# Optimization experiments

Measured on AMD Instinct MI355X. Metric: run time of the kernel, lower is better.

Reference implementation:

```python
import jax, jax.numpy as jnp
import numpy as np

# ---- fixed problem dimensions ----
B, S, T = 64, 200, 32          # batch of sequences, trees per seq, nodes per tree
V, E, C = 50000, 128, 128      # vocab, embedding_dim, encode_dim
H, OUT = 100, 104              # GRU hidden, output_dim
N = B * S * T                  # total nodes
D_MAX = 5                      # max depth of a 32-node complete binary tree


def setup_inputs() -> dict:
    key = jax.random.key(0)
    ks = jax.random.split(key, 16)
    # --- tree structure: every tree is a complete binary tree with T nodes ---
    local_parent = np.array([0] + [(i - 1) // 2 for i in range(1, T)], dtype=np.int64)
    local_depth = np.array([int(np.floor(np.log2(i + 1))) for i in range(T)], dtype=np.int64)
    num_trees = B * S
    offsets = np.arange(num_trees, dtype=np.int64) * T
    node_parent = (offsets[:, None] + local_parent[None, :]).reshape(-1)
    node_depth = np.tile(local_depth, num_trees)
    node_tree = np.repeat(np.arange(num_trees, dtype=np.int64), T)
    node_tokens = jax.random.randint(ks[0], (N,), 0, V, dtype=jnp.int64)
    sc = 0.05
    inp = {
        "node_tokens": node_tokens,
        "node_parent": jnp.asarray(node_parent),
        "node_tree": jnp.asarray(node_tree),
        "node_depth": jnp.asarray(node_depth),
        "emb": jax.random.normal(ks[1], (V, E), jnp.float32) * sc,
        "w_lin": jax.random.normal(ks[2], (C, E), jnp.float32) * sc,
        "b_lin": jnp.zeros((C,), jnp.float32),
        "w_ih_f": jax.random.normal(ks[3], (3 * H, C), jnp.float32) * sc,
        "w_hh_f": jax.random.normal(ks[4], (3 * H, H), jnp.float32) * sc,
        "b_ih_f": jnp.zeros((3 * H,), jnp.float32),
        "b_hh_f": jnp.zeros((3 * H,), jnp.float32),
        "w_ih_b": jax.random.normal(ks[5], (3 * H, C), jnp.float32) * sc,
        "w_hh_b": jax.random.normal(ks[6], (3 * H, H), jnp.float32) * sc,
        "b_ih_b": jnp.zeros((3 * H,), jnp.float32),
        "b_hh_b": jnp.zeros((3 * H,), jnp.float32),
        "fc_w": jax.random.normal(ks[7], (OUT, 2 * H), jnp.float32) * sc,
        "fc_b": jnp.zeros((OUT,), jnp.float32),
    }
    return inp


def _gru(x_sbc, w_ih, w_hh, b_ih, b_hh):
    """Torch-convention GRU over leading time axis. x_sbc: [S, B, C] -> [S, B, H]."""
    h0 = jnp.zeros((x_sbc.shape[1], w_hh.shape[1]), x_sbc.dtype)

    def step(h, xt):
        gx = xt @ w_ih.T + b_ih
        gh = h @ w_hh.T + b_hh
        xr, xz, xn = jnp.split(gx, 3, axis=-1)
        hr, hz, hn = jnp.split(gh, 3, axis=-1)
        r = jax.nn.sigmoid(xr + hr)
        z = jax.nn.sigmoid(xz + hz)
        n = jnp.tanh(xn + r * hn)
        h_new = (1.0 - z) * n + z * h
        return h_new, h_new

    _, hs = jax.lax.scan(step, h0, x_sbc)
    return hs


def reference(node_tokens, node_parent, node_tree, node_depth,
              emb, w_lin, b_lin,
              w_ih_f, w_hh_f, b_ih_f, b_hh_f,
              w_ih_b, w_hh_b, b_ih_b, b_hh_b,
              fc_w, fc_b):
    # per-node contribution: W * emb(token) + b   (recursion base of hidden_state)
    c = emb[node_tokens] @ w_lin.T + b_lin               # [N, C]
    # level-batched bottom-up scatter-add: h(node) = c(node) + sum(h(children))
    h = c
    for d in range(D_MAX, 0, -1):
        mask = (node_depth == d)[:, None]
        h = h.at[node_parent].add(jnp.where(mask, h, 0.0))
    # per-tree max pool over all node hidden states (TreeEncoder output)
    tree_vec = jax.ops.segment_max(h, node_tree, num_segments=B * S)  # [B*S, C]
    x = tree_vec.reshape(B, S, C)
    # bidirectional GRU (batch_first in torch; scan over time here)
    x_t = jnp.transpose(x, (1, 0, 2))                    # [S, B, C]
    fwd = _gru(x_t, w_ih_f, w_hh_f, b_ih_f, b_hh_f)      # [S, B, H]
    bwd = _gru(x_t[::-1], w_ih_b, w_hh_b, b_ih_b, b_hh_b)[::-1]
    gru_out = jnp.concatenate([fwd, bwd], axis=-1)       # [S, B, 2H]
    pool = gru_out.max(axis=0)                           # [B, 2H] (max over time)
    return pool @ fc_w.T + fc_b                          # [B, OUT]
```

## Files before the change

### kernel.cpp

```cpp
#include <hip/hip_runtime.h>
#include <hip/hip_bf16.h>
#include <math.h>

#define BB 64
#define SS 200
#define TT 32
#define VV 50000
#define EE 128
#define CC 128
#define HH 100
#define G3 300
#define OUTD 104
#define NTREE (BB*SS)

typedef __attribute__((ext_vector_type(4))) float f32x4;
typedef _Float16 f16x8 __attribute__((ext_vector_type(8)));

#define L2E  1.4426950408889634f
#define NL2E (-1.4426950408889634f)
#define TL2E 2.8853900817779268f

#define BAR() asm volatile("s_waitcnt lgkmcnt(0)\n\ts_barrier" ::: "memory")


__global__ __launch_bounds__(256) void k0_prep(const float* __restrict__ w_lin,
                                               const float* __restrict__ w_ih_f,
                                               const float* __restrict__ w_ih_b,
                                               const float* __restrict__ emb,
                                               _Float16* __restrict__ wl,
                                               _Float16* __restrict__ k2b,
                                               _Float16* __restrict__ emb16) {
    const int tid  = threadIdx.x;
    const int wave = tid >> 6;
    const int lane = tid & 63;
    const int r = lane & 15;
    const int q = lane >> 4;
    if (blockIdx.x == 0) {
#pragma unroll
        for (int nt = 0; nt < 2; ++nt)
#pragma unroll
            for (int kt = 0; kt < 4; ++kt) {
                const int n = wave * 32 + nt * 16 + r;
                const float* src = w_lin + (long)n * EE + kt * 32 + q * 8;
                f16x8 f;
#pragma unroll
                for (int e = 0; e < 8; ++e) f[e] = (_Float16)src[e];
                *(f16x8*)&wl[(size_t)((((wave * 2 + nt) * 4 + kt) * 64) + lane) * 8] = f;
            }
    } else if (blockIdx.x <= 10) {
        const int nb = blockIdx.x - 1;
        const int n = nb * 64 + wave * 16 + r;
        const int dir = (n >= 320) ? 1 : 0;
        const int j = n - dir * 320;
        const int jj = (j < G3) ? j : 0;
        const float* w = dir ? w_ih_b : w_ih_f;
#pragma unroll
        for (int kt = 0; kt < 4; ++kt) {
            const float* src = w + (long)jj * EE + kt * 32 + q * 8;
            f16x8 f;
#pragma unroll
            for (int e = 0; e < 8; ++e) f[e] = (_Float16)src[e];
            *(f16x8*)&k2b[(size_t)((((nb * 4 + wave) * 4 + kt) * 64) + lane) * 8] = f;
        }
    } else {
        const long base = (long)(blockIdx.x - 11) * 2048 + (long)tid * 8;
        if (base < (long)VV * EE) {
            const float4* s = (const float4*)(emb + base);
            const float4 v0 = s[0], v1 = s[1];
            f16x8 f;
            f[0] = (_Float16)v0.x; f[1] = (_Float16)v0.y;
            f[2] = (_Float16)v0.z; f[3] = (_Float16)v0.w;
            f[4] = (_Float16)v1.x; f[5] = (_Float16)v1.y;
            f[6] = (_Float16)v1.z; f[7] = (_Float16)v1.w;
            *(f16x8*)&emb16[base] = f;
        }
    }
}

#define K1_TPI 2
#define AROWS (K1_TPI*TT)
#define LDA 136
#define LDC 132

__global__ __launch_bounds__(256, 4) void k1_mfma(const int* __restrict__ tok,
                                                  const _Float16* __restrict__ emb16,
                                                  const _Float16* __restrict__ wl,
                                                  const float* __restrict__ b_lin,
                                                  _Float16* __restrict__ thi) {
    __shared__ __align__(16) char U_sh[AROWS * LDC * 4];
    _Float16* A_sh = (_Float16*)U_sh;
    float*    C_sh = (float*)U_sh;
    __shared__ int tok_sh[AROWS];

    const int tid  = threadIdx.x;
    const int wave = tid >> 6;
    const int lane = tid & 63;
    const int r = lane & 15;
    const int q = lane >> 4;

    f16x8 bfrag[2][4];
    float bias[2];
#pragma unroll
    for (int nt = 0; nt < 2; ++nt) {
        bias[nt] = b_lin[wave * 32 + nt * 16 + r];
#pragma unroll
        for (int kt = 0; kt < 4; ++kt)
            bfrag[nt][kt] = *(const f16x8*)&wl[(size_t)((((wave * 2 + nt) * 4 + kt) * 64) + lane) * 8];
    }

    const int tree0 = blockIdx.x * K1_TPI;
    if (tid < AROWS) tok_sh[tid] = tok[tree0 * TT + tid];
    __syncthreads();

#pragma unroll
    for (int i = 0; i < 4; ++i) {
        const int idx = tid + i * 256;
        const int row = idx >> 4;
        const int p   = idx & 15;
        const f16x8 v = *(const f16x8*)&emb16[(long)tok_sh[row] * EE + p * 8];
        *(f16x8*)&A_sh[row * LDA + p * 8] = v;
    }
    __syncthreads();

    f32x4 acc[4][2];
#pragma unroll
    for (int mt = 0; mt < 4; ++mt)
#pragma unroll
        for (int nt = 0; nt < 2; ++nt) acc[mt][nt] = (f32x4)(0.f);

#pragma unroll
    for (int mt = 0; mt < 4; ++mt) {
        const int m = mt * 16 + r;
        f16x8 afrag[4];
#pragma unroll
        for (int kt = 0; kt < 4; ++kt)
            afrag[kt] = *(const f16x8*)&A_sh[m * LDA + kt * 32 + q * 8];
#pragma unroll
        for (int nt = 0; nt < 2; ++nt)
#pragma unroll
            for (int kt = 0; kt < 4; ++kt)
                acc[mt][nt] = __builtin_amdgcn_mfma_f32_16x16x32_f16(
                    afrag[kt], bfrag[nt][kt], acc[mt][nt], 0, 0, 0);
    }
    __syncthreads();

#pragma unroll
    for (int mt = 0; mt < 4; ++mt)
#pragma unroll
        for (int nt = 0; nt < 2; ++nt) {
            const int col = wave * 32 + nt * 16 + r;
#pragma unroll
            for (int reg = 0; reg < 4; ++reg) {
                const int row = mt * 16 + q * 4 + reg;
                C_sh[row * LDC + col] = acc[mt][nt][reg] + bias[nt];
            }
        }
    __syncthreads();

    {
        const int t = tid >> 7;
        const int j = tid & 127;
        const float* base = &C_sh[(t * TT) * LDC + j];
        float v[TT];
#pragma unroll
        for (int n = 0; n < TT; ++n) v[n] = base[n * LDC];
        float mx = -1e30f;
#pragma unroll
        for (int n = TT - 1; n >= 1; --n) {
            mx = fmaxf(mx, v[n]);
            v[(n - 1) >> 1] += v[n];
        }
        mx = fmaxf(mx, v[0]);
        thi[(size_t)(tree0 + t) * CC + j] = (_Float16)mx;
    }
}

__global__ __launch_bounds__(256) void k2_mfma(const _Float16* __restrict__ thi,
                                               const _Float16* __restrict__ k2b,
                                               const float* __restrict__ b_ih_f,
                                               const float* __restrict__ b_ih_b,
                                               const float* __restrict__ b_hh_f,
                                               const float* __restrict__ b_hh_b,
                                               float* __restrict__ gx) {
    __shared__ __align__(16) _Float16 Ah[64 * LDA];

    const int tid  = threadIdx.x;
    const int wave = tid >> 6;
    const int lane = tid & 63;
    const int r = lane & 15;
    const int q = lane >> 4;

    const int nbp = blockIdx.x % 5;
    const int mb2 = blockIdx.x / 5;
    const int m0 = mb2 * 64;

#pragma unroll
    for (int i = 0; i < 4; ++i) {
        const int idx = tid + i * 256;
        const int row = idx >> 4;
        const int p   = idx & 15;
        f16x8 v = *(const f16x8*)&thi[(size_t)(m0 + row) * CC + p * 8];
        *(f16x8*)&Ah[row * LDA + p * 8] = v;
    }
    f16x8 bh[2][4];
#pragma unroll
    for (int i = 0; i < 2; ++i) {
        const int nb = nbp + i * 5;
#pragma unroll
        for (int kt = 0; kt < 4; ++kt)
            bh[i][kt] = *(const f16x8*)&k2b[(size_t)((((nb * 4 + wave) * 4 + kt) * 64) + lane) * 8];
    }
    __syncthreads();

    f32x4 acc[2][4];
#pragma unroll
    for (int i = 0; i < 2; ++i)
#pragma unroll
        for (int mt = 0; mt < 4; ++mt) acc[i][mt] = (f32x4)(0.f);

#pragma unroll
    for (int mt = 0; mt < 4; ++mt) {
        const int m = mt * 16 + r;
        f16x8 a[4];
#pragma unroll
        for (int kt = 0; kt < 4; ++kt)
            a[kt] = *(const f16x8*)&Ah[m * LDA + kt * 32 + q * 8];
#pragma unroll
        for (int i = 0; i < 2; ++i)
#pragma unroll
            for (int kt = 0; kt < 4; ++kt)
                acc[i][mt] = __builtin_amdgcn_mfma_f32_16x16x32_f16(a[kt], bh[i][kt], acc[i][mt], 0, 0, 0);
    }

#pragma unroll
    for (int i = 0; i < 2; ++i) {
        const int ng  = (nbp + i * 5) * 64 + wave * 16 + r;
        const int dir = (ng >= 320) ? 1 : 0;
        const int j   = ng - dir * 320;
        const bool valid = (j < G3);
        const float* b_ih = dir ? b_ih_b : b_ih_f;
        const float* b_hh = dir ? b_hh_b : b_hh_f;
        const float bias = valid ? b_ih[j] : 0.f;
        const float bh2  = (valid && j < 2 * HH) ? b_hh[j] : 0.f;
        const float sc   = (j < 2 * HH) ? NL2E : TL2E;
        float* gxd = gx + (long)dir * NTREE * G3;
        if (valid) {
#pragma unroll
            for (int mt = 0; mt < 4; ++mt)
#pragma unroll
                for (int reg = 0; reg < 4; ++reg) {
                    const int m = m0 + mt * 16 + q * 4 + reg;
                    gxd[(long)m * G3 + j] = sc * (acc[i][mt][reg] + bias + bh2);
                }
        }
    }
}

__global__ __launch_bounds__(256, 1) void k3_gru(const float* __restrict__ gx,
                                                 const float* __restrict__ w_hh_f,
                                                 const float* __restrict__ b_hh_f,
                                                 const float* __restrict__ w_hh_b,
                                                 const float* __restrict__ b_hh_b,
                                                 float* __restrict__ pool) {
    const int bid = blockIdx.x;
    const int dir = bid & 1;
    const int b = bid >> 1;
    const float* w_hh = dir ? w_hh_b : w_hh_f;
    const float* b_hh = dir ? b_hh_b : b_hh_f;

    __shared__ __align__(16) _Float16 h_sh[2][128];

    const int tid  = threadIdx.x;
    const int wave = tid >> 6;
    const int lane = tid & 63;
    const int r = lane & 15;
    const int q = lane >> 4;

    f16x8 bf[5][4];
#pragma unroll
    for (int i = 0; i < 5; ++i) {
        const int l = i * 16 + r;
        const int gate = l / 25;
        const int ch   = l - gate * 25;
        const bool nv  = (l < 75);
        const int row  = gate * HH + wave * 25 + ch;
        const float sc = (gate == 2) ? TL2E : NL2E;
#pragma unroll
        for (int kt = 0; kt < 4; ++kt) {
            f16x8 f;
#pragma unroll
            for (int e = 0; e < 8; ++e) {
                const int k = kt * 32 + q * 8 + e;
                f[e] = (_Float16)((nv && k < HH) ? sc * w_hh[row * HH + k] : 0.f);
            }
            bf[i][kt] = f;
        }
    }

    const int m = lane;
    const int c = wave * 25 + m;
    const bool act = (m < 25);
    const float bnc = act ? TL2E * b_hh[2 * HH + c] : 0.f;

    const int a_z  = (25 + m) & 63;
    const int a_n1 = (50 + m) & 63;
    const int a_n2 = (50 + m - 64) & 63;
    const bool nV1 = (50 + m) < 64;

    if (tid < 128) { h_sh[0][tid] = (_Float16)0.f; h_sh[1][tid] = (_Float16)0.f; }

    const int sstep = dir ? -1 : 1;
    const int s0 = dir ? (SS - 1) : 0;
    const float* gp = gx + (long)dir * NTREE * G3 + (long)b * SS * G3 + c;

    float pxr[4], pxz[4], pxn[4];
    if (act) {
#pragma unroll
        for (int j = 0; j < 4; ++j) {
            const long off = (long)(s0 + j * sstep) * G3;
            pxr[j] = gp[off]; pxz[j] = gp[off + HH]; pxn[j] = gp[off + 2 * HH];
        }
    }
    float hj = 0.f, hmax = -1e30f;
    __syncthreads();

    int s = s0;
    for (int t = 0; t < SS; t += 4) {
#pragma unroll
        for (int j = 0; j < 4; ++j) {
            const int p = j & 1;

            f16x8 a[4];
#pragma unroll
            for (int kt = 0; kt < 4; ++kt)
                a[kt] = *(const f16x8*)&h_sh[p][kt * 32 + q * 8];

            f32x4 accA[5], accB[5];
#pragma unroll
            for (int i = 0; i < 5; ++i) {
                accA[i] = (f32x4)(0.f);
                accB[i] = (f32x4)(0.f);
                accA[i] = __builtin_amdgcn_mfma_f32_16x16x32_f16(a[0], bf[i][0], accA[i], 0, 0, 0);
                accB[i] = __builtin_amdgcn_mfma_f32_16x16x32_f16(a[2], bf[i][2], accB[i], 0, 0, 0);
                accA[i] = __builtin_amdgcn_mfma_f32_16x16x32_f16(a[1], bf[i][1], accA[i], 0, 0, 0);
                accB[i] = __builtin_amdgcn_mfma_f32_16x16x32_f16(a[3], bf[i][3], accB[i], 0, 0, 0);
            }
            const float g0 = accA[0][0] + accB[0][0];
            const float g1 = accA[1][0] + accB[1][0];
            const float g2 = accA[2][0] + accB[2][0];
            const float g3 = accA[3][0] + accB[3][0];
            const float g4 = accA[4][0] + accB[4][0];
            float V1 = g0;
            V1 = (q == 1) ? g1 : V1;
            V1 = (q == 2) ? g2 : V1;
            V1 = (q == 3) ? g3 : V1;
            const float ghr = V1;
            const float ghz = __shfl(V1, a_z);
            const float vnA = __shfl(V1, a_n1);
            const float vnB = __shfl(g4, a_n2);
            const float ghn = nV1 ? vnA : vnB;

            if (act) {
                const float rg = __builtin_amdgcn_rcpf(1.f + __builtin_amdgcn_exp2f(pxr[j] + ghr));
                const float zg = __builtin_amdgcn_rcpf(1.f + __builtin_amdgcn_exp2f(pxz[j] + ghz));
                const float t1 = ghn + bnc;
                const float an = __builtin_fmaf(rg, t1, pxn[j]);
                const float u  = __builtin_amdgcn_rcpf(1.f + __builtin_amdgcn_exp2f(an));
                const float n  = __builtin_fmaf(-2.f, u, 1.f);
                hj = __builtin_fmaf(zg, hj - n, n);
                h_sh[1 - p][c] = (_Float16)hj;
                hmax = fmaxf(hmax, hj);
                if (t + j + 4 < SS) {
                    const long off = (long)(s + (j + 4) * sstep) * G3;
                    pxr[j] = gp[off]; pxz[j] = gp[off + HH]; pxn[j] = gp[off + 2 * HH];
                }
            }
            BAR();
        }
        s += 4 * sstep;
    }
    if (act) pool[(long)b * (2 * HH) + dir * HH + c] = hmax;
}

__global__ __launch_bounds__(256) void k4_fc(const float* __restrict__ pool,
                                             const float* __restrict__ fc_w,
                                             const float* __restrict__ fc_b,
                                             float* __restrict__ out) {
    const int b = blockIdx.x;
    __shared__ __align__(16) float p_sh[2 * HH];
    const int t = threadIdx.x;
    if (t < 2 * HH) p_sh[t] = pool[(long)b * (2 * HH) + t];
    __syncthreads();
    if (t < OUTD) {
        const float4* wr4 = (const float4*)(fc_w + (long)t * (2 * HH));
        const float4* p4 = (const float4*)p_sh;
        float a0 = 0.f, a1 = 0.f;
#pragma unroll
        for (int k = 0; k < 50; k += 2) {
            float4 w0 = wr4[k],   p0 = p4[k];
            float4 w1 = wr4[k+1], p1 = p4[k+1];
            a0 += w0.x*p0.x + w0.y*p0.y + w0.z*p0.z + w0.w*p0.w;
            a1 += w1.x*p1.x + w1.y*p1.y + w1.z*p1.z + w1.w*p1.w;
        }
        out[(long)b * OUTD + t] = fc_b[t] + a0 + a1;
    }
}

extern "C" void kernel_launch(void* const* d_in, const int* in_sizes, int n_in,
                              void* d_out, int out_size, void* d_ws, size_t ws_size,
                              hipStream_t stream) {
    const int*   tok    = (const int*)d_in[0];
    const float* emb    = (const float*)d_in[4];
    const float* w_lin  = (const float*)d_in[5];
    const float* b_lin  = (const float*)d_in[6];
    const float* w_ih_f = (const float*)d_in[7];
    const float* w_hh_f = (const float*)d_in[8];
    const float* b_ih_f = (const float*)d_in[9];
    const float* b_hh_f = (const float*)d_in[10];
    const float* w_ih_b = (const float*)d_in[11];
    const float* w_hh_b = (const float*)d_in[12];
    const float* b_ih_b = (const float*)d_in[13];
    const float* b_hh_b = (const float*)d_in[14];
    const float* fc_w   = (const float*)d_in[15];
    const float* fc_b   = (const float*)d_in[16];

    char* wsb = (char*)d_ws;
    _Float16* wl    = (_Float16*)(wsb);
    _Float16* k2b   = (_Float16*)(wsb + 32768);
    _Float16* thi   = (_Float16*)(wsb + 196608);
    float*    gx    = (float*)(wsb + 3473408);
    _Float16* emb16 = (_Float16*)(wsb + 3473408);
    float*    pool  = (float*)(wsb);
    float*    out   = (float*)d_out;

    k0_prep<<<11 + 3125, 256, 0, stream>>>(w_lin, w_ih_f, w_ih_b, emb, wl, k2b, emb16);
    k1_mfma<<<NTREE / K1_TPI, 256, 0, stream>>>(tok, emb16, wl, b_lin, thi);
    k2_mfma<<<(NTREE / 64) * 5, 256, 0, stream>>>(thi, k2b, b_ih_f, b_ih_b,
                                                  b_hh_f, b_hh_b, gx);
    k3_gru <<<2 * BB, 256, 0, stream>>>(gx, w_hh_f, b_hh_f, w_hh_b, b_hh_b, pool);
    k4_fc  <<<BB, 256, 0, stream>>>(pool, fc_w, fc_b, out);
}
```

Before: 229.2 us.

## Precompute projected embedding table per vocab row and gather instead of per-node GEMM

```diff
diff --git a/kernel.cpp b/kernel.cpp
--- a/kernel.cpp
+++ b/kernel.cpp
@@ -23,32 +23,25 @@
 #define BAR() asm volatile("s_waitcnt lgkmcnt(0)\n\ts_barrier" ::: "memory")
 
 
+#define LDA 136
+#define AROWS 64
+
 __global__ __launch_bounds__(256) void k0_prep(const float* __restrict__ w_lin,
                                                const float* __restrict__ w_ih_f,
                                                const float* __restrict__ w_ih_b,
                                                const float* __restrict__ emb,
-                                               _Float16* __restrict__ wl,
+                                               const float* __restrict__ b_lin,
                                                _Float16* __restrict__ k2b,
-                                               _Float16* __restrict__ emb16) {
+                                               float* __restrict__ ctab) {
+    __shared__ __align__(16) _Float16 A_sh[AROWS * LDA];
     const int tid  = threadIdx.x;
     const int wave = tid >> 6;
     const int lane = tid & 63;
     const int r = lane & 15;
     const int q = lane >> 4;
-    if (blockIdx.x == 0) {
-#pragma unroll
-        for (int nt = 0; nt < 2; ++nt)
-#pragma unroll
-            for (int kt = 0; kt < 4; ++kt) {
-                const int n = wave * 32 + nt * 16 + r;
-                const float* src = w_lin + (long)n * EE + kt * 32 + q * 8;
-                f16x8 f;
-#pragma unroll
-                for (int e = 0; e < 8; ++e) f[e] = (_Float16)src[e];
-                *(f16x8*)&wl[(size_t)((((wave * 2 + nt) * 4 + kt) * 64) + lane) * 8] = f;
-            }
-    } else if (blockIdx.x <= 10) {
-        const int nb = blockIdx.x - 1;
+
+    if (blockIdx.x < 10) {
+        const int nb = blockIdx.x;
         const int n = nb * 64 + wave * 16 + r;
         const int dir = (n >= 320) ? 1 : 0;
         const int j = n - dir * 320;
@@ -62,63 +55,38 @@
             for (int e = 0; e < 8; ++e) f[e] = (_Float16)src[e];
             *(f16x8*)&k2b[(size_t)((((nb * 4 + wave) * 4 + kt) * 64) + lane) * 8] = f;
         }
-    } else {
-        const long base = (long)(blockIdx.x - 11) * 2048 + (long)tid * 8;
-        if (base < (long)VV * EE) {
-            const float4* s = (const float4*)(emb + base);
-            const float4 v0 = s[0], v1 = s[1];
-            f16x8 f;
-            f[0] = (_Float16)v0.x; f[1] = (_Float16)v0.y;
-            f[2] = (_Float16)v0.z; f[3] = (_Float16)v0.w;
-            f[4] = (_Float16)v1.x; f[5] = (_Float16)v1.y;
-            f[6] = (_Float16)v1.z; f[7] = (_Float16)v1.w;
-            *(f16x8*)&emb16[base] = f;
-        }
-    }
-}
-
-#define K1_TPI 2
-#define AROWS (K1_TPI*TT)
-#define LDA 136
-#define LDC 132
-
-__global__ __launch_bounds__(256, 4) void k1_mfma(const int* __restrict__ tok,
-                                                  const _Float16* __restrict__ emb16,
-                                                  const _Float16* __restrict__ wl,
-                                                  const float* __restrict__ b_lin,
-                                                  _Float16* __restrict__ thi) {
-    __shared__ __align__(16) char U_sh[AROWS * LDC * 4];
-    _Float16* A_sh = (_Float16*)U_sh;
-    float*    C_sh = (float*)U_sh;
-    __shared__ int tok_sh[AROWS];
-
-    const int tid  = threadIdx.x;
-    const int wave = tid >> 6;
-    const int lane = tid & 63;
-    const int r = lane & 15;
-    const int q = lane >> 4;
+        return;
+    }
+
+    const int row0 = (blockIdx.x - 10) * 64;
 
     f16x8 bfrag[2][4];
     float bias[2];
 #pragma unroll
     for (int nt = 0; nt < 2; ++nt) {
-        bias[nt] = b_lin[wave * 32 + nt * 16 + r];
-#pragma unroll
-        for (int kt = 0; kt < 4; ++kt)
-            bfrag[nt][kt] = *(const f16x8*)&wl[(size_t)((((wave * 2 + nt) * 4 + kt) * 64) + lane) * 8];
-    }
-
-    const int tree0 = blockIdx.x * K1_TPI;
-    if (tid < AROWS) tok_sh[tid] = tok[tree0 * TT + tid];
-    __syncthreads();
-
-#pragma unroll
-    for (int i = 0; i < 4; ++i) {
+        const int n = wave * 32 + nt * 16 + r;
+        bias[nt] = b_lin[n];
+#pragma unroll
+        for (int kt = 0; kt < 4; ++kt) {
+            const float* src = w_lin + (long)n * EE + kt * 32 + q * 8;
+            f16x8 f;
+#pragma unroll
+            for (int e = 0; e < 8; ++e) f[e] = (_Float16)src[e];
+            bfrag[nt][kt] = f;
+        }
+    }
+
+#pragma unroll
+    for (int i = 0; i < 8; ++i) {
         const int idx = tid + i * 256;
-        const int row = idx >> 4;
-        const int p   = idx & 15;
-        const f16x8 v = *(const f16x8*)&emb16[(long)tok_sh[row] * EE + p * 8];
-        *(f16x8*)&A_sh[row * LDA + p * 8] = v;
+        const int row = idx >> 5;
+        const int p   = idx & 31;
+        const int gr  = row0 + row;
+        const int grc = (gr < VV) ? gr : (VV - 1);
+        const float4 e = ((const float4*)(emb + (long)grc * EE))[p];
+        _Float16* dst = &A_sh[row * LDA + p * 4];
+        dst[0] = (_Float16)e.x; dst[1] = (_Float16)e.y;
+        dst[2] = (_Float16)e.z; dst[3] = (_Float16)e.w;
     }
     __syncthreads();
 
@@ -142,7 +110,6 @@
                 acc[mt][nt] = __builtin_amdgcn_mfma_f32_16x16x32_f16(
                     afrag[kt], bfrag[nt][kt], acc[mt][nt], 0, 0, 0);
     }
-    __syncthreads();
 
 #pragma unroll
     for (int mt = 0; mt < 4; ++mt)
@@ -151,28 +118,39 @@
             const int col = wave * 32 + nt * 16 + r;
 #pragma unroll
             for (int reg = 0; reg < 4; ++reg) {
-                const int row = mt * 16 + q * 4 + reg;
-                C_sh[row * LDC + col] = acc[mt][nt][reg] + bias[nt];
+                const int gr = row0 + mt * 16 + q * 4 + reg;
+                if (gr < VV)
+                    ctab[(long)gr * CC + col] = acc[mt][nt][reg] + bias[nt];
             }
         }
+}
+
+__global__ __launch_bounds__(256) void k1_gather(const int* __restrict__ tok,
+                                                 const float* __restrict__ ctab,
+                                                 _Float16* __restrict__ thi) {
+    __shared__ int tok_sh[64];
+    const int tid = threadIdx.x;
+    const int tree0 = blockIdx.x * 2;
+    if (tid < 64) tok_sh[tid] = tok[tree0 * TT + tid];
     __syncthreads();
 
-    {
-        const int t = tid >> 7;
-        const int j = tid & 127;
-        const float* base = &C_sh[(t * TT) * LDC + j];
-        float v[TT];
-#pragma unroll
-        for (int n = 0; n < TT; ++n) v[n] = base[n * LDC];
-        float mx = -1e30f;
-#pragma unroll
-        for (int n = TT - 1; n >= 1; --n) {
-            mx = fmaxf(mx, v[n]);
-            v[(n - 1) >> 1] += v[n];
-        }
-        mx = fmaxf(mx, v[0]);
-        thi[(size_t)(tree0 + t) * CC + j] = (_Float16)mx;
-    }
+    const int t = tid >> 7;
+    const int j = tid & 127;
+    const int* tk = &tok_sh[t * TT];
+
+    float v[TT];
+#pragma unroll
+    for (int n = 0; n < TT; ++n)
+        v[n] = ctab[(long)tk[n] * CC + j];
+
+    float mx = -1e30f;
+#pragma unroll
+    for (int n = TT - 1; n >= 1; --n) {
+        mx = fmaxf(mx, v[n]);
+        v[(n - 1) >> 1] += v[n];
+    }
+    mx = fmaxf(mx, v[0]);
+    thi[(size_t)(tree0 + t) * CC + j] = (_Float16)mx;
 }
 
 __global__ __launch_bounds__(256) void k2_mfma(const _Float16* __restrict__ thi,
@@ -425,18 +403,18 @@
     const float* fc_b   = (const float*)d_in[16];
 
     char* wsb = (char*)d_ws;
-    _Float16* wl    = (_Float16*)(wsb);
-    _Float16* k2b   = (_Float16*)(wsb + 32768);
-    _Float16* thi   = (_Float16*)(wsb + 196608);
-    float*    gx    = (float*)(wsb + 3473408);
-    _Float16* emb16 = (_Float16*)(wsb + 3473408);
-    float*    pool  = (float*)(wsb);
-    float*    out   = (float*)d_out;
-
-    k0_prep<<<11 + 3125, 256, 0, stream>>>(w_lin, w_ih_f, w_ih_b, emb, wl, k2b, emb16);
-    k1_mfma<<<NTREE / K1_TPI, 256, 0, stream>>>(tok, emb16, wl, b_lin, thi);
-    k2_mfma<<<(NTREE / 64) * 5, 256, 0, stream>>>(thi, k2b, b_ih_f, b_ih_b,
-                                                  b_hh_f, b_hh_b, gx);
-    k3_gru <<<2 * BB, 256, 0, stream>>>(gx, w_hh_f, b_hh_f, w_hh_b, b_hh_b, pool);
-    k4_fc  <<<BB, 256, 0, stream>>>(pool, fc_w, fc_b, out);
-}
+    _Float16* k2b  = (_Float16*)(wsb + 32768);
+    _Float16* thi  = (_Float16*)(wsb + 196608);
+    float*    gx   = (float*)(wsb + 3473408);
+    float*    ctab = (float*)(wsb + 3473408);
+    float*    pool = (float*)(wsb);
+    float*    out  = (float*)d_out;
+
+    k0_prep  <<<10 + (VV + 63) / 64, 256, 0, stream>>>(w_lin, w_ih_f, w_ih_b, emb,
+                                                       b_lin, k2b, ctab);
+    k1_gather<<<NTREE / 2, 256, 0, stream>>>(tok, ctab, thi);
+    k2_mfma  <<<(NTREE / 64) * 5, 256, 0, stream>>>(thi, k2b, b_ih_f, b_ih_b,
+                                                    b_hh_f, b_hh_b, gx);
+    k3_gru   <<<2 * BB, 256, 0, stream>>>(gx, w_hh_f, b_hh_f, w_hh_b, b_hh_b, pool);
+    k4_fc    <<<BB, 256, 0, stream>>>(pool, fc_w, fc_b, out);
+}
```

Result: slower. 244.8 us (+6.8%).
